# Kernel optimization log

Hardware: AMD Instinct MI355X
Metric: run time of the kernel (lower is better)

## Reference

```python
import jax, jax.numpy as jnp
import numpy as np

N_NODES = 200000
N_EDGES = 800000
HID = 256
OUT = 4
IN = 6


def setup_inputs() -> dict:
    key = jax.random.key(0)
    ks = jax.random.split(key, 32)
    s = 0.05  # weight scale for numerical sanity
    inp = {
        'x': jax.random.normal(ks[0], (N_NODES, 10), dtype=jnp.float32),
        'edge_index': jax.random.randint(ks[1], (2, N_EDGES), 0, N_NODES, dtype=jnp.int64),
        'w1': jax.random.normal(ks[2], (IN, HID), jnp.float32) * s,
        'b1': jnp.zeros((HID,), jnp.float32),
        'w2': jax.random.normal(ks[3], (HID, OUT), jnp.float32) * s,
        'b2': jnp.zeros((OUT,), jnp.float32),
        'e1': jax.random.normal(ks[4], (IN, HID), jnp.float32) * s,
        'be1': jnp.zeros((HID,), jnp.float32),
        'e2': jax.random.normal(ks[5], (HID, HID), jnp.float32) * s,
        'be2': jnp.zeros((HID,), jnp.float32),
    }
    for l, od in enumerate([HID, HID, HID, OUT]):
        inp[f'rw{l}'] = jax.random.normal(ks[6 + 3 * l], (HID, od), jnp.float32) * s
        inp[f'rb{l}'] = jnp.zeros((od,), jnp.float32)
        inp[f'sw{l}'] = jax.random.normal(ks[7 + 3 * l], (HID, od), jnp.float32) * s
    return inp


def _graph_conv(h, src, tgt, Wr, br, Ws, n):
    # PyG GraphConv (aggr='add'): out_i = W_rel @ sum_{j->i} h_j + b_rel + W_root @ h_i
    agg = jax.ops.segment_sum(h[src], tgt, num_segments=n)  # [N, d_in]
    return agg @ Wr + br + h @ Ws


def reference(x, edge_index, w1, b1, w2, b2, e1, be1, e2, be2,
              rw0, rb0, sw0, rw1, rb1, sw1, rw2, rb2, sw2, rw3, rb3, sw3):
    n = x.shape[0]
    src, tgt = edge_index[0], edge_index[1]
    xs = x[:, 4:10]  # x_start=4, x_end=10 -> in_dim=6

    # weak MLP expert
    weak = jax.nn.relu(xs @ w1 + b1) @ w2 + b2  # [N, OUT]

    # strong GNN expert
    h = jax.nn.relu(xs @ e1 + be1) @ e2 + be2  # [N, HID]
    h = jax.nn.relu(_graph_conv(h, src, tgt, rw0, rb0, sw0, n))
    h = jax.nn.relu(_graph_conv(h, src, tgt, rw1, rb1, sw1, n))
    h = jax.nn.relu(_graph_conv(h, src, tgt, rw2, rb2, sw2, n))
    strong = _graph_conv(h, src, tgt, rw3, rb3, sw3, n)  # [N, OUT]

    # dispersion-based confidence gate
    probs = jax.nn.softmax(weak, axis=-1)
    var = jnp.var(probs, axis=-1)  # unbiased=False
    ent = -jnp.sum(probs * jnp.log(probs + 1e-8), axis=-1)
    ent = ent / jnp.log(jnp.float32(probs.shape[-1]))
    conf = jnp.clip(0.5 * (var + (1.0 - ent)), 0.0, 1.0)

    return conf[:, None] * weak + (1.0 - conf[:, None]) * strong
```

## Files before the change

### kernel.cpp

```cpp
#include <hip/hip_runtime.h>
#include <hip/hip_bf16.h>
#include <hip/hip_fp16.h>

#define NN 200000
#define NE 800000
#define HID 256
#define SCAN_NBLK 196

typedef __attribute__((ext_vector_type(8))) _Float16 f16x8;
typedef __attribute__((ext_vector_type(4))) float    f32x4;

__device__ __forceinline__ float2 upk(unsigned int u) {
    __half2 h = __builtin_bit_cast(__half2, u);
    return make_float2(__low2float(h), __high2float(h));
}
__device__ __forceinline__ unsigned int pk(float a, float b) {
    __half2 h = __floats2half2_rn(a, b);
    return __builtin_bit_cast(unsigned int, h);
}

__device__ __forceinline__ float bfu(unsigned short u) {
    return __uint_as_float(((unsigned int)u) << 16);
}
__device__ __forceinline__ unsigned short f2bf(float f) {
    unsigned int u = __float_as_uint(f);
    return (unsigned short)((u + 0x7FFFu + ((u >> 16) & 1u)) >> 16);
}
__device__ __forceinline__ float ldF(const void* p, size_t i, int bf) {
    return bf ? bfu(((const unsigned short*)p)[i]) : ((const float*)p)[i];
}
__device__ __forceinline__ float4 ld4(const void* p, size_t i, int bf) {
    if (bf) {
        ushort4 u = *reinterpret_cast<const ushort4*>((const unsigned short*)p + i);
        return make_float4(bfu(u.x), bfu(u.y), bfu(u.z), bfu(u.w));
    }
    return *reinterpret_cast<const float4*>((const float*)p + i);
}
__device__ __forceinline__ void ld8(const void* p, size_t i, int bf, float* v) {
    if (bf) {
        ushort4 u0 = *reinterpret_cast<const ushort4*>((const unsigned short*)p + i);
        ushort4 u1 = *reinterpret_cast<const ushort4*>((const unsigned short*)p + i + 4);
        v[0] = bfu(u0.x); v[1] = bfu(u0.y); v[2] = bfu(u0.z); v[3] = bfu(u0.w);
        v[4] = bfu(u1.x); v[5] = bfu(u1.y); v[6] = bfu(u1.z); v[7] = bfu(u1.w);
    } else {
        float4 a = *reinterpret_cast<const float4*>((const float*)p + i);
        float4 b = *reinterpret_cast<const float4*>((const float*)p + i + 4);
        v[0] = a.x; v[1] = a.y; v[2] = a.z; v[3] = a.w;
        v[4] = b.x; v[5] = b.y; v[6] = b.z; v[7] = b.w;
    }
}
__device__ __forceinline__ int ldE(const int* ei, size_t i, int i64) {
    return i64 ? ei[2 * i] : ei[i];
}

__global__ void detect_kernel(const void* x, const int* ei, int* flags)
{
    if (threadIdx.x == 0 && blockIdx.x == 0) {
        const unsigned short* xu = (const unsigned short*)x;
        int good = 0;
        for (int k = 0; k < 128; ++k) {
            float a = fabsf(bfu(xu[2 * k]));
            if (a == 0.f || (a >= 9.3e-10f && a <= 64.f)) ++good;
        }
        flags[0] = (good >= 64) ? 1 : 0;
        int zeros = 0;
        for (int k = 0; k < 128; ++k)
            if (ei[2 * k + 1] == 0) ++zeros;
        flags[1] = (zeros >= 64) ? 1 : 0;
    }
}

__global__ __launch_bounds__(256) void prepT256_kernel(
    const void* __restrict__ W, const int* __restrict__ flags, __half* __restrict__ WT)
{
    const int bf = flags[0];
    int id = blockIdx.x * 256 + threadIdx.x;
    int k = id & 255, n = id >> 8;
    WT[(size_t)n * 256 + k] = __float2half_rn(ldF(W, (size_t)k * 256 + n, bf));
}

__global__ __launch_bounds__(256) void prepT512_kernel(
    const void* __restrict__ Rw, const void* __restrict__ Sw,
    const int* __restrict__ flags, __half* __restrict__ WT)
{
    const int bf = flags[0];
    int id = blockIdx.x * 256 + threadIdx.x;
    int k = id & 511, n = id >> 9;
    const void* src = (k < 256) ? Rw : Sw;
    WT[(size_t)n * 512 + k] = __float2half_rn(ldF(src, (size_t)(k & 255) * 256 + n, bf));
}

__global__ __launch_bounds__(256) void prepW8_kernel(
    const void* __restrict__ rw3, const void* __restrict__ sw3,
    const int* __restrict__ flags, __half* __restrict__ W8T)
{
    const int bf = flags[0];
    int id = blockIdx.x * 256 + threadIdx.x;
    int c = id >> 8, k = id & 255;
    float v = 0.f;
    if (c < 4)      v = ldF(rw3, (size_t)k * 4 + c, bf);
    else if (c < 8) v = ldF(sw3, (size_t)k * 4 + (c - 4), bf);
    W8T[(size_t)c * 256 + k] = __float2half_rn(v);
}

__global__ __launch_bounds__(256) void frontT_kernel(
    const void* __restrict__ x,
    const void* __restrict__ e1, const void* __restrict__ be1,
    const int* __restrict__ flags, __half* __restrict__ T)
{
    const int bf = flags[0];
    const int t = threadIdx.x;
    const int wave = t >> 6, lane = t & 63;
    const int half = lane >> 5, l32 = lane & 31;
    const int j0 = l32 * 8;

    float ev[6][8], be[8];
    ld8(be1, j0, bf, be);
#pragma unroll
    for (int k = 0; k < 6; ++k) ld8(e1, (size_t)k * HID + j0, bf, ev[k]);

    const int slot = blockIdx.x * 4 + wave;
    const int nslots = gridDim.x * 4;
    for (int n = slot * 2 + half; n < NN; n += nslots * 2) {
        float xs[6];
#pragma unroll
        for (int k = 0; k < 6; ++k) xs[k] = ldF(x, (size_t)n * 10 + 4 + k, bf);
        float a[8];
#pragma unroll
        for (int jj = 0; jj < 8; ++jj) a[jj] = be[jj];
#pragma unroll
        for (int k = 0; k < 6; ++k)
#pragma unroll
            for (int jj = 0; jj < 8; ++jj)
                a[jj] = fmaf(xs[k], ev[k][jj], a[jj]);
        uint4 o;
        o.x = pk(fmaxf(a[0], 0.f), fmaxf(a[1], 0.f));
        o.y = pk(fmaxf(a[2], 0.f), fmaxf(a[3], 0.f));
        o.z = pk(fmaxf(a[4], 0.f), fmaxf(a[5], 0.f));
        o.w = pk(fmaxf(a[6], 0.f), fmaxf(a[7], 0.f));
        *reinterpret_cast<uint4*>(&T[(size_t)n * HID + j0]) = o;
    }
}

__global__ __launch_bounds__(256) void frontW_kernel(
    const void* __restrict__ x,
    const void* __restrict__ w1, const void* __restrict__ b1,
    const void* __restrict__ w2, const void* __restrict__ b2,
    const int* __restrict__ flags, float* __restrict__ weakO)
{
    const int bf = flags[0];
    const int t = threadIdx.x;
    const int wave = t >> 6, lane = t & 63;
    const int half = lane >> 5, l32 = lane & 31;
    const int j0 = l32 * 8;

    float wv[6][8], bb[8], w2r[8][4];
    ld8(b1, j0, bf, bb);
#pragma unroll
    for (int k = 0; k < 6; ++k) ld8(w1, (size_t)k * HID + j0, bf, wv[k]);
#pragma unroll
    for (int jj = 0; jj < 8; ++jj) {
        float4 r = ld4(w2, (size_t)(j0 + jj) * 4, bf);
        w2r[jj][0] = r.x; w2r[jj][1] = r.y; w2r[jj][2] = r.z; w2r[jj][3] = r.w;
    }
    float b2v[4];
#pragma unroll
    for (int c = 0; c < 4; ++c) b2v[c] = ldF(b2, c, bf);

    const int slot = blockIdx.x * 4 + wave;
    const int nslots = gridDim.x * 4;
    for (int n = slot * 2 + half; n < NN; n += nslots * 2) {
        float xs[6];
#pragma unroll
        for (int k = 0; k < 6; ++k) xs[k] = ldF(x, (size_t)n * 10 + 4 + k, bf);
        float a[8];
#pragma unroll
        for (int jj = 0; jj < 8; ++jj) a[jj] = bb[jj];
#pragma unroll
        for (int k = 0; k < 6; ++k)
#pragma unroll
            for (int jj = 0; jj < 8; ++jj)
                a[jj] = fmaf(xs[k], wv[k][jj], a[jj]);
        float wa[4] = {0.f, 0.f, 0.f, 0.f};
#pragma unroll
        for (int jj = 0; jj < 8; ++jj) {
            float av = fmaxf(a[jj], 0.f);
#pragma unroll
            for (int c = 0; c < 4; ++c) wa[c] = fmaf(av, w2r[jj][c], wa[c]);
        }
#pragma unroll
        for (int off = 16; off >= 1; off >>= 1)
#pragma unroll
            for (int c = 0; c < 4; ++c) wa[c] += __shfl_xor(wa[c], off);
        if (l32 == 0) {
            float4 w = {wa[0] + b2v[0], wa[1] + b2v[1], wa[2] + b2v[2], wa[3] + b2v[3]};
            *reinterpret_cast<float4*>(&weakO[(size_t)n * 4]) = w;
        }
    }
}

template<int KTOT, int RELU>
__global__ __launch_bounds__(512) void mfma_gemm_kernel(
    const __half* A0, const __half* __restrict__ A1,
    const __half* __restrict__ WT, const void* __restrict__ bias,
    const int* __restrict__ flags, __half* OUT)
{
    const int bf = flags[0];
    __shared__ alignas(16) __half As[128 * 32];
    __shared__ alignas(16) __half Ws[256 * 32];

    const int t    = threadIdx.x;
    const int bm   = blockIdx.x * 128;
    const int lane = t & 63;
    const int w    = t >> 6;
    const int wr   = w >> 2, wc = w & 3;
    const int lr   = lane & 15, lg = lane >> 4;

    f32x4 acc[4][4] = {};

    for (int k0 = 0; k0 < KTOT; k0 += 32) {
        __syncthreads();
        {
            const __half* src = (KTOT == 512 && k0 >= 256) ? A1 : A0;
            const int kk0 = k0 & 255;
            int row = t >> 2, c = t & 3;
            int gm = bm + row;
            uint4 v = make_uint4(0, 0, 0, 0);
            if (gm < NN)
                v = *reinterpret_cast<const uint4*>(&src[(size_t)gm * HID + kk0 + c * 8]);
            int sc = c ^ ((row >> 1) & 3);
            *reinterpret_cast<uint4*>(&As[row * 32 + sc * 8]) = v;
        }
#pragma unroll
        for (int p = 0; p < 2; ++p) {
            int cid = p * 512 + t;
            int n = cid >> 2, c = cid & 3;
            uint4 v = *reinterpret_cast<const uint4*>(&WT[(size_t)n * KTOT + k0 + c * 8]);
            int sc = c ^ ((n >> 1) & 3);
            *reinterpret_cast<uint4*>(&Ws[n * 32 + sc * 8]) = v;
        }
        __syncthreads();

        f16x8 a[4], b[4];
#pragma unroll
        for (int i = 0; i < 4; ++i) {
            int row = wr * 64 + i * 16 + lr;
            int sc = lg ^ ((row >> 1) & 3);
            a[i] = *reinterpret_cast<const f16x8*>(&As[row * 32 + sc * 8]);
        }
#pragma unroll
        for (int j = 0; j < 4; ++j) {
            int n = wc * 64 + j * 16 + lr;
            int sc = lg ^ ((n >> 1) & 3);
            b[j] = *reinterpret_cast<const f16x8*>(&Ws[n * 32 + sc * 8]);
        }
#pragma unroll
        for (int i = 0; i < 4; ++i)
#pragma unroll
            for (int j = 0; j < 4; ++j)
                acc[i][j] = __builtin_amdgcn_mfma_f32_16x16x32_f16(a[i], b[j], acc[i][j], 0, 0, 0);
    }

    float bv[4];
#pragma unroll
    for (int j = 0; j < 4; ++j) bv[j] = ldF(bias, wc * 64 + j * 16 + lr, bf);
#pragma unroll
    for (int i = 0; i < 4; ++i) {
        int rowBase = bm + wr * 64 + i * 16 + lg * 4;
#pragma unroll
        for (int r = 0; r < 4; ++r) {
            int gr = rowBase + r;
            if (gr < NN) {
#pragma unroll
                for (int j = 0; j < 4; ++j) {
                    int col = wc * 64 + j * 16 + lr;
                    float v = acc[i][j][r] + bv[j];
                    if (RELU) v = fmaxf(v, 0.f);
                    OUT[(size_t)gr * HID + col] = __float2half_rn(v);
                }
            }
        }
    }
}

__global__ __launch_bounds__(256) void zeroI_kernel(int* __restrict__ p, int n)
{
    int i = blockIdx.x * 256 + threadIdx.x;
    if (i < n) p[i] = 0;
}

__global__ __launch_bounds__(256) void count_kernel(
    const int* __restrict__ ei, const int* __restrict__ flags, int* __restrict__ rowptr)
{
    const int i64 = flags[1];
    int e = blockIdx.x * 256 + threadIdx.x;
    if (e >= NE) return;
    int tgt = ldE(ei, (size_t)NE + e, i64);
    if ((unsigned)tgt < NN) atomicAdd(&rowptr[tgt + 1], 1);
}

__global__ __launch_bounds__(256) void scanA_kernel(
    const int* __restrict__ rowptr, int* __restrict__ partials)
{
    __shared__ int red[256];
    const int b = blockIdx.x, t = threadIdx.x;
    int base = b * 1024 + t * 4;
    int s = 0;
#pragma unroll
    for (int k = 0; k < 4; ++k) {
        int i = base + k;
        if (i <= NN) s += rowptr[i];
    }
    red[t] = s;
    __syncthreads();
    for (int off = 128; off >= 1; off >>= 1) {
        if (t < off) red[t] += red[t + off];
        __syncthreads();
    }
    if (t == 0) partials[b] = red[0];
}

__global__ __launch_bounds__(256) void scanB_kernel(int* __restrict__ partials)
{
    __shared__ int ps[256];
    const int t = threadIdx.x;
    int v = (t < SCAN_NBLK) ? partials[t] : 0;
    ps[t] = v;
    __syncthreads();
    for (int off = 1; off < 256; off <<= 1) {
        int u = (t >= off) ? ps[t - off] : 0;
        __syncthreads();
        ps[t] += u;
        __syncthreads();
    }
    if (t < SCAN_NBLK) partials[t] = ps[t] - v;
}

__global__ __launch_bounds__(256) void scanC_kernel(
    int* __restrict__ rowptr, const int* __restrict__ partials)
{
    __shared__ int ts[256];
    const int b = blockIdx.x, t = threadIdx.x;
    int base = b * 1024 + t * 4;
    int v[4];
    int s = 0;
#pragma unroll
    for (int k = 0; k < 4; ++k) {
        int i = base + k;
        v[k] = (i <= NN) ? rowptr[i] : 0;
        s += v[k];
    }
    ts[t] = s;
    __syncthreads();
    for (int off = 1; off < 256; off <<= 1) {
        int u = (t >= off) ? ts[t - off] : 0;
        __syncthreads();
        ts[t] += u;
        __syncthreads();
    }
    int run = ts[t] - s + partials[b];
#pragma unroll
    for (int k = 0; k < 4; ++k) {
        int i = base + k;
        run += v[k];
        if (i <= NN) rowptr[i] = run;
    }
}

__global__ __launch_bounds__(256) void fill_kernel(
    const int* __restrict__ ei, const int* __restrict__ flags,
    const int* __restrict__ rowptr, int* __restrict__ cursor, int* __restrict__ csr_src)
{
    const int i64 = flags[1];
    int e = blockIdx.x * 256 + threadIdx.x;
    if (e >= NE) return;
    int src = ldE(ei, (size_t)e, i64);
    int tgt = ldE(ei, (size_t)NE + e, i64);
    if ((unsigned)src >= NN || (unsigned)tgt >= NN) return;
    int pos = rowptr[tgt] + atomicAdd(&cursor[tgt], 1);
    csr_src[pos] = src;
}

__global__ __launch_bounds__(256) void gather_kernel(
    const int* __restrict__ rowptr, const int* __restrict__ csr_src,
    const __half* __restrict__ H, __half* __restrict__ AGG)
{
    int n = blockIdx.x * 4 + (threadIdx.x >> 6);
    int lane = threadIdx.x & 63;
    if (n >= NN) return;
    int beg = rowptr[n], end = rowptr[n + 1];
    float a0 = 0.f, a1 = 0.f, a2 = 0.f, a3 = 0.f;
    for (int j = beg; j < end; ++j) {
        int s = csr_src[j];
        uint2 q = *reinterpret_cast<const uint2*>(&H[(size_t)s * HID + lane * 4]);
        float2 lo = upk(q.x), hi = upk(q.y);
        a0 += lo.x; a1 += lo.y; a2 += hi.x; a3 += hi.y;
    }
    uint2 o;
    o.x = pk(a0, a1);
    o.y = pk(a2, a3);
    *reinterpret_cast<uint2*>(&AGG[(size_t)n * HID + lane * 4]) = o;
}

__global__ __launch_bounds__(256) void gemv3_mfma_kernel(
    const __half* __restrict__ h, const __half* __restrict__ W8T,
    const void* __restrict__ rb3, const int* __restrict__ flags,
    float* __restrict__ B3, float* __restrict__ C3)
{
    const int bf = flags[0];
    __shared__ alignas(16) __half As[128 * 32];

    const int t    = threadIdx.x;
    const int bm   = blockIdx.x * 128;
    const int lane = t & 63;
    const int w    = t >> 6;
    const int lr   = lane & 15, lg = lane >> 4;

    f32x4 acc[2] = {};

    for (int k0 = 0; k0 < HID; k0 += 32) {
        __syncthreads();
#pragma unroll
        for (int p = 0; p < 2; ++p) {
            int cid = p * 256 + t;
            int row = cid >> 2, c = cid & 3;
            int gm = bm + row;
            uint4 v = make_uint4(0, 0, 0, 0);
            if (gm < NN)
                v = *reinterpret_cast<const uint4*>(&h[(size_t)gm * HID + k0 + c * 8]);
            int sc = c ^ ((row >> 1) & 3);
            *reinterpret_cast<uint4*>(&As[row * 32 + sc * 8]) = v;
        }
        __syncthreads();

        f16x8 b = *reinterpret_cast<const f16x8*>(&W8T[(size_t)lr * HID + k0 + lg * 8]);
#pragma unroll
        for (int i = 0; i < 2; ++i) {
            int row = w * 32 + i * 16 + lr;
            int sc = lg ^ ((row >> 1) & 3);
            f16x8 a = *reinterpret_cast<const f16x8*>(&As[row * 32 + sc * 8]);
            acc[i] = __builtin_amdgcn_mfma_f32_16x16x32_f16(a, b, acc[i], 0, 0, 0);
        }
    }

    float rbv = (lr >= 4 && lr < 8) ? ldF(rb3, lr - 4, bf) : 0.f;
#pragma unroll
    for (int i = 0; i < 2; ++i) {
        int rowBase = bm + w * 32 + i * 16 + lg * 4;
#pragma unroll
        for (int r = 0; r < 4; ++r) {
            int gr = rowBase + r;
            if (gr < NN) {
                float v = acc[i][r];
                if (lr < 4)      B3[(size_t)gr * 4 + lr] = v;
                else if (lr < 8) C3[(size_t)gr * 4 + (lr - 4)] = v + rbv;
            }
        }
    }
}

__global__ __launch_bounds__(256) void gather3_kernel(
    const int* __restrict__ rowptr, const int* __restrict__ csr_src,
    const float* __restrict__ B3, float* __restrict__ C3)
{
    int n = blockIdx.x * 256 + threadIdx.x;
    if (n >= NN) return;
    int beg = rowptr[n], end = rowptr[n + 1];
    float4 acc = *reinterpret_cast<const float4*>(&C3[(size_t)n * 4]);
    for (int j = beg; j < end; ++j) {
        int s = csr_src[j];
        float4 v = *reinterpret_cast<const float4*>(&B3[(size_t)s * 4]);
        acc.x += v.x; acc.y += v.y; acc.z += v.z; acc.w += v.w;
    }
    *reinterpret_cast<float4*>(&C3[(size_t)n * 4]) = acc;
}

__global__ __launch_bounds__(256) void final_kernel(
    const float* __restrict__ weakO, const float* __restrict__ strongO,
    const int* __restrict__ flags, void* __restrict__ outv)
{
    const int bf = flags[0];
    int n = blockIdx.x * 256 + threadIdx.x;
    if (n >= NN) return;
    float4 w = *reinterpret_cast<const float4*>(&weakO[(size_t)n * 4]);
    float4 s = *reinterpret_cast<const float4*>(&strongO[(size_t)n * 4]);
    float mx = fmaxf(fmaxf(w.x, w.y), fmaxf(w.z, w.w));
    float e0 = expf(w.x - mx), e1 = expf(w.y - mx), e2 = expf(w.z - mx), e3 = expf(w.w - mx);
    float inv = 1.f / (e0 + e1 + e2 + e3);
    float p0 = e0 * inv, p1 = e1 * inv, p2 = e2 * inv, p3 = e3 * inv;
    const float m = 0.25f;
    float var = ((p0 - m) * (p0 - m) + (p1 - m) * (p1 - m) +
                 (p2 - m) * (p2 - m) + (p3 - m) * (p3 - m)) * 0.25f;
    float ent = -(p0 * logf(p0 + 1e-8f) + p1 * logf(p1 + 1e-8f) +
                  p2 * logf(p2 + 1e-8f) + p3 * logf(p3 + 1e-8f));
    ent *= 0.7213475204444817f;
    float conf = 0.5f * (var + (1.f - ent));
    conf = fminf(fmaxf(conf, 0.f), 1.f);
    float o0 = conf * w.x + (1.f - conf) * s.x;
    float o1 = conf * w.y + (1.f - conf) * s.y;
    float o2 = conf * w.z + (1.f - conf) * s.z;
    float o3 = conf * w.w + (1.f - conf) * s.w;
    if (bf) {
        ushort4 u;
        u.x = f2bf(o0); u.y = f2bf(o1); u.z = f2bf(o2); u.w = f2bf(o3);
        *reinterpret_cast<ushort4*>((unsigned short*)outv + (size_t)n * 4) = u;
    } else {
        float4 o = {o0, o1, o2, o3};
        *reinterpret_cast<float4*>((float*)outv + (size_t)n * 4) = o;
    }
}

extern "C" void kernel_launch(void* const* d_in, const int* in_sizes, int n_in,
                              void* d_out, int out_size, void* d_ws, size_t ws_size,
                              hipStream_t stream)
{
    const void* x   = d_in[0];
    const int*  ei  = (const int*)d_in[1];
    const void* w1  = d_in[2];
    const void* b1  = d_in[3];
    const void* w2  = d_in[4];
    const void* b2  = d_in[5];
    const void* e1  = d_in[6];
    const void* be1 = d_in[7];
    const void* e2  = d_in[8];
    const void* be2 = d_in[9];
    const void* rw[4] = {d_in[10], d_in[13], d_in[16], d_in[19]};
    const void* rb[4] = {d_in[11], d_in[14], d_in[17], d_in[20]};
    const void* sw[4] = {d_in[12], d_in[15], d_in[18], d_in[21]};

    char* base = (char*)d_ws;
    size_t off = 0;
    auto alloc = [&](size_t bytes) { char* p = base + off; off += (bytes + 255) & ~(size_t)255; return p; };
    int*    flags   = (int*)alloc(64 * 4);
    int*    rowptr  = (int*)alloc((size_t)(NN + 1) * 4);
    int*    cursor  = (int*)alloc((size_t)NN * 4);
    int*    csr_src = (int*)alloc((size_t)NE * 4);
    int*    partials= (int*)alloc((size_t)SCAN_NBLK * 4);
    float*  weakP   = (float*)alloc((size_t)NN * 4 * 4);
    float*  B3      = (float*)alloc((size_t)NN * 4 * 4);
    float*  C3      = (float*)alloc((size_t)NN * 4 * 4);
    __half* e2T     = (__half*)alloc((size_t)256 * 256 * 2);
    __half* wcatT   = (__half*)alloc((size_t)3 * 256 * 512 * 2);
    __half* W8T     = (__half*)alloc((size_t)16 * 256 * 2);
    __half* buf0    = (__half*)alloc((size_t)NN * HID * 2);
    __half* buf1    = (__half*)alloc((size_t)NN * HID * 2);

    if (ws_size && off > ws_size) {
        hipMemsetAsync(d_out, 0, (size_t)out_size * 2, stream);
        return;
    }

    const int gGemm = 1563;
    const int gEdge = (NE + 255) / 256;
    const int gNode1 = (NN + 255) / 256;

    detect_kernel<<<1, 64, 0, stream>>>(x, ei, flags);

    prepT256_kernel<<<256, 256, 0, stream>>>(e2, flags, e2T);
    prepT512_kernel<<<512, 256, 0, stream>>>(rw[0], sw[0], flags, wcatT);
    prepT512_kernel<<<512, 256, 0, stream>>>(rw[1], sw[1], flags, wcatT + (size_t)256 * 512);
    prepT512_kernel<<<512, 256, 0, stream>>>(rw[2], sw[2], flags, wcatT + (size_t)2 * 256 * 512);
    prepW8_kernel<<<16, 256, 0, stream>>>(rw[3], sw[3], flags, W8T);

    zeroI_kernel<<<(NN + 1 + 255) / 256, 256, 0, stream>>>(rowptr, NN + 1);
    zeroI_kernel<<<gNode1, 256, 0, stream>>>(cursor, NN);
    count_kernel<<<gEdge, 256, 0, stream>>>(ei, flags, rowptr);
    scanA_kernel<<<SCAN_NBLK, 256, 0, stream>>>(rowptr, partials);
    scanB_kernel<<<1, 256, 0, stream>>>(partials);
    scanC_kernel<<<SCAN_NBLK, 256, 0, stream>>>(rowptr, partials);
    fill_kernel<<<gEdge, 256, 0, stream>>>(ei, flags, rowptr, cursor, csr_src);

    frontT_kernel<<<2048, 256, 0, stream>>>(x, e1, be1, flags, buf0);
    frontW_kernel<<<2048, 256, 0, stream>>>(x, w1, b1, w2, b2, flags, weakP);

    mfma_gemm_kernel<256, 0><<<gGemm, 512, 0, stream>>>(buf0, nullptr, e2T, be2, flags, buf1);

    gather_kernel<<<50000, 256, 0, stream>>>(rowptr, csr_src, buf1, buf0);
    mfma_gemm_kernel<512, 1><<<gGemm, 512, 0, stream>>>(buf0, buf1, wcatT, rb[0], flags, buf0);

    gather_kernel<<<50000, 256, 0, stream>>>(rowptr, csr_src, buf0, buf1);
    mfma_gemm_kernel<512, 1><<<gGemm, 512, 0, stream>>>(buf1, buf0, wcatT + (size_t)256 * 512, rb[1], flags, buf1);

    gather_kernel<<<50000, 256, 0, stream>>>(rowptr, csr_src, buf1, buf0);
    mfma_gemm_kernel<512, 1><<<gGemm, 512, 0, stream>>>(buf0, buf1, wcatT + (size_t)2 * 256 * 512, rb[2], flags, buf0);

    gemv3_mfma_kernel<<<gGemm, 256, 0, stream>>>(buf0, W8T, rb[3], flags, B3, C3);
    gather3_kernel<<<gNode1, 256, 0, stream>>>(rowptr, csr_src, B3, C3);

    final_kernel<<<gNode1, 256, 0, stream>>>(weakP, C3, flags, d_out);
}
```

Measured before the change: 842.7 us.

## Fuse neighbor gather into GraphConv GEMM via shared-memory aggregation tile

Replaces the separate gather kernel and 512-K GEMM per conv layer with one fused kernel. Each 64-row block first aggregates its neighbor sums directly into a swizzled shared-memory tile, then runs the MFMA GEMM over the aggregated half and the root half of H. This removes the write and re-read of the AGG buffer to global memory for each layer. In exchange, blocks are smaller (64 rows, 4 waves) and use more LDS, and the weight tile is reloaded per 64 rows instead of per 128. The gather phase also serializes within each wave, which can lower occupancy and latency hiding.

New measurement: 1.161 ms. 37.8% more time.

```diff
diff --git a/kernel.cpp b/kernel.cpp
--- a/kernel.cpp
+++ b/kernel.cpp
@@ -199,11 +199,9 @@
     }
 }
 
-template<int KTOT, int RELU>
 __global__ __launch_bounds__(512) void mfma_gemm_kernel(
-    const __half* A0, const __half* __restrict__ A1,
-    const __half* __restrict__ WT, const void* __restrict__ bias,
-    const int* __restrict__ flags, __half* OUT)
+    const __half* __restrict__ A0, const __half* __restrict__ WT,
+    const void* __restrict__ bias, const int* __restrict__ flags, __half* __restrict__ OUT)
 {
     const int bf = flags[0];
     __shared__ alignas(16) __half As[128 * 32];
@@ -218,16 +216,14 @@
 
     f32x4 acc[4][4] = {};
 
-    for (int k0 = 0; k0 < KTOT; k0 += 32) {
+    for (int k0 = 0; k0 < 256; k0 += 32) {
         __syncthreads();
         {
-            const __half* src = (KTOT == 512 && k0 >= 256) ? A1 : A0;
-            const int kk0 = k0 & 255;
             int row = t >> 2, c = t & 3;
             int gm = bm + row;
             uint4 v = make_uint4(0, 0, 0, 0);
             if (gm < NN)
-                v = *reinterpret_cast<const uint4*>(&src[(size_t)gm * HID + kk0 + c * 8]);
+                v = *reinterpret_cast<const uint4*>(&A0[(size_t)gm * HID + k0 + c * 8]);
             int sc = c ^ ((row >> 1) & 3);
             *reinterpret_cast<uint4*>(&As[row * 32 + sc * 8]) = v;
         }
@@ -235,7 +231,7 @@
         for (int p = 0; p < 2; ++p) {
             int cid = p * 512 + t;
             int n = cid >> 2, c = cid & 3;
-            uint4 v = *reinterpret_cast<const uint4*>(&WT[(size_t)n * KTOT + k0 + c * 8]);
+            uint4 v = *reinterpret_cast<const uint4*>(&WT[(size_t)n * 256 + k0 + c * 8]);
             int sc = c ^ ((n >> 1) & 3);
             *reinterpret_cast<uint4*>(&Ws[n * 32 + sc * 8]) = v;
         }
@@ -274,8 +270,109 @@
 #pragma unroll
                 for (int j = 0; j < 4; ++j) {
                     int col = wc * 64 + j * 16 + lr;
-                    float v = acc[i][j][r] + bv[j];
-                    if (RELU) v = fmaxf(v, 0.f);
+                    OUT[(size_t)gr * HID + col] = __float2half_rn(acc[i][j][r] + bv[j]);
+                }
+            }
+        }
+    }
+}
+
+__global__ __launch_bounds__(256, 3) void conv_fused_kernel(
+    const __half* __restrict__ H, const int* __restrict__ rowptr,
+    const int* __restrict__ csr_src, const __half* __restrict__ WT,
+    const void* __restrict__ rb, const int* __restrict__ flags,
+    __half* __restrict__ OUT)
+{
+    const int bf = flags[0];
+    __shared__ alignas(16) __half AggS[8 * 2080];
+    __shared__ alignas(16) __half Ws[256 * 32];
+    __shared__ alignas(16) __half AsH[64 * 32];
+
+    const int t    = threadIdx.x;
+    const int bm   = blockIdx.x * 64;
+    const int lane = t & 63;
+    const int w    = t >> 6;
+    const int lr   = lane & 15, lg = lane >> 4;
+
+    {
+        const int gg = lane >> 3, cc = (lane >> 1) & 3, sub = (lane & 1) * 4;
+#pragma unroll 1
+        for (int rr = w * 16; rr < w * 16 + 16; ++rr) {
+            int n = bm + rr;
+            float a0 = 0.f, a1 = 0.f, a2 = 0.f, a3 = 0.f;
+            if (n < NN) {
+                int beg = rowptr[n], end = rowptr[n + 1];
+                for (int j = beg; j < end; ++j) {
+                    int s = csr_src[j];
+                    uint2 q = *reinterpret_cast<const uint2*>(&H[(size_t)s * HID + lane * 4]);
+                    float2 lo = upk(q.x), hi = upk(q.y);
+                    a0 += lo.x; a1 += lo.y; a2 += hi.x; a3 += hi.y;
+                }
+            }
+            int sc = cc ^ ((rr >> 1) & 3);
+            uint2 o; o.x = pk(a0, a1); o.y = pk(a2, a3);
+            *reinterpret_cast<uint2*>(&AggS[gg * 2080 + rr * 32 + sc * 8 + sub]) = o;
+        }
+    }
+
+    f32x4 acc[4][4] = {};
+    for (int g = 0; g < 16; ++g) {
+        __syncthreads();
+#pragma unroll
+        for (int p = 0; p < 4; ++p) {
+            int cid = p * 256 + t;
+            int n = cid >> 2, c = cid & 3;
+            uint4 v = *reinterpret_cast<const uint4*>(&WT[(size_t)n * 512 + g * 32 + c * 8]);
+            int sc = c ^ ((n >> 1) & 3);
+            *reinterpret_cast<uint4*>(&Ws[n * 32 + sc * 8]) = v;
+        }
+        if (g >= 8) {
+            int row = t >> 2, c = t & 3;
+            int gm = bm + row;
+            uint4 v = make_uint4(0, 0, 0, 0);
+            if (gm < NN)
+                v = *reinterpret_cast<const uint4*>(&H[(size_t)gm * HID + (g - 8) * 32 + c * 8]);
+            int sc = c ^ ((row >> 1) & 3);
+            *reinterpret_cast<uint4*>(&AsH[row * 32 + sc * 8]) = v;
+        }
+        __syncthreads();
+
+        f16x8 a[4], b[4];
+#pragma unroll
+        for (int i = 0; i < 4; ++i) {
+            int row = i * 16 + lr;
+            int sc = lg ^ ((row >> 1) & 3);
+            a[i] = (g < 8)
+                 ? *reinterpret_cast<const f16x8*>(&AggS[g * 2080 + row * 32 + sc * 8])
+                 : *reinterpret_cast<const f16x8*>(&AsH[row * 32 + sc * 8]);
+        }
+#pragma unroll
+        for (int j = 0; j < 4; ++j) {
+            int n = w * 64 + j * 16 + lr;
+            int sc = lg ^ ((n >> 1) & 3);
+            b[j] = *reinterpret_cast<const f16x8*>(&Ws[n * 32 + sc * 8]);
+        }
+#pragma unroll
+        for (int i = 0; i < 4; ++i)
+#pragma unroll
+            for (int j = 0; j < 4; ++j)
+                acc[i][j] = __builtin_amdgcn_mfma_f32_16x16x32_f16(a[i], b[j], acc[i][j], 0, 0, 0);
+    }
+
+    float bv[4];
+#pragma unroll
+    for (int j = 0; j < 4; ++j) bv[j] = ldF(rb, w * 64 + j * 16 + lr, bf);
+#pragma unroll
+    for (int i = 0; i < 4; ++i) {
+        int rowBase = bm + i * 16 + lg * 4;
+#pragma unroll
+        for (int r = 0; r < 4; ++r) {
+            int gr = rowBase + r;
+            if (gr < NN) {
+#pragma unroll
+                for (int j = 0; j < 4; ++j) {
+                    int col = w * 64 + j * 16 + lr;
+                    float v = fmaxf(acc[i][j][r] + bv[j], 0.f);
                     OUT[(size_t)gr * HID + col] = __float2half_rn(v);
                 }
             }
@@ -379,27 +476,6 @@
     if ((unsigned)src >= NN || (unsigned)tgt >= NN) return;
     int pos = rowptr[tgt] + atomicAdd(&cursor[tgt], 1);
     csr_src[pos] = src;
-}
-
-__global__ __launch_bounds__(256) void gather_kernel(
-    const int* __restrict__ rowptr, const int* __restrict__ csr_src,
-    const __half* __restrict__ H, __half* __restrict__ AGG)
-{
-    int n = blockIdx.x * 4 + (threadIdx.x >> 6);
-    int lane = threadIdx.x & 63;
-    if (n >= NN) return;
-    int beg = rowptr[n], end = rowptr[n + 1];
-    float a0 = 0.f, a1 = 0.f, a2 = 0.f, a3 = 0.f;
-    for (int j = beg; j < end; ++j) {
-        int s = csr_src[j];
-        uint2 q = *reinterpret_cast<const uint2*>(&H[(size_t)s * HID + lane * 4]);
-        float2 lo = upk(q.x), hi = upk(q.y);
-        a0 += lo.x; a1 += lo.y; a2 += hi.x; a3 += hi.y;
-    }
-    uint2 o;
-    o.x = pk(a0, a1);
-    o.y = pk(a2, a3);
-    *reinterpret_cast<uint2*>(&AGG[(size_t)n * HID + lane * 4]) = o;
 }
 
 __global__ __launch_bounds__(256) void gemv3_mfma_kernel(
@@ -550,7 +626,7 @@
         return;
     }
 
-    const int gGemm = 1563;
+    const int gConv = 3125;
     const int gEdge = (NE + 255) / 256;
     const int gNode1 = (NN + 255) / 256;
 
@@ -573,18 +649,13 @@
     frontT_kernel<<<2048, 256, 0, stream>>>(x, e1, be1, flags, buf0);
     frontW_kernel<<<2048, 256, 0, stream>>>(x, w1, b1, w2, b2, flags, weakP);
 
-    mfma_gemm_kernel<256, 0><<<gGemm, 512, 0, stream>>>(buf0, nullptr, e2T, be2, flags, buf1);
-
-    gather_kernel<<<50000, 256, 0, stream>>>(rowptr, csr_src, buf1, buf0);
-    mfma_gemm_kernel<512, 1><<<gGemm, 512, 0, stream>>>(buf0, buf1, wcatT, rb[0], flags, buf0);
-
-    gather_kernel<<<50000, 256, 0, stream>>>(rowptr, csr_src, buf0, buf1);
-    mfma_gemm_kernel<512, 1><<<gGemm, 512, 0, stream>>>(buf1, buf0, wcatT + (size_t)256 * 512, rb[1], flags, buf1);
-
-    gather_kernel<<<50000, 256, 0, stream>>>(rowptr, csr_src, buf1, buf0);
-    mfma_gemm_kernel<512, 1><<<gGemm, 512, 0, stream>>>(buf0, buf1, wcatT + (size_t)2 * 256 * 512, rb[2], flags, buf0);
-
-    gemv3_mfma_kernel<<<gGemm, 256, 0, stream>>>(buf0, W8T, rb[3], flags, B3, C3);
+    mfma_gemm_kernel<<<1563, 512, 0, stream>>>(buf0, e2T, be2, flags, buf1);
+
+    conv_fused_kernel<<<gConv, 256, 0, stream>>>(buf1, rowptr, csr_src, wcatT, rb[0], flags, buf0);
+    conv_fused_kernel<<<gConv, 256, 0, stream>>>(buf0, rowptr, csr_src, wcatT + (size_t)256 * 512, rb[1], flags, buf1);
+    conv_fused_kernel<<<gConv, 256, 0, stream>>>(buf1, rowptr, csr_src, wcatT + (size_t)2 * 256 * 512, rb[2], flags, buf0);
+
+    gemv3_mfma_kernel<<<1563, 256, 0, stream>>>(buf0, W8T, rb[3], flags, B3, C3);
     gather3_kernel<<<gNode1, 256, 0, stream>>>(rowptr, csr_src, B3, C3);
 
     final_kernel<<<gNode1, 256, 0, stream>>>(weakP, C3, flags, d_out);
```
